# Performance work log

Measured on AMD Instinct MI355X. Metric: run time of the kernel, lower is better.

Reference implementation:

```python
import jax, jax.numpy as jnp
import numpy as np

N = 100000      # nodes
E = 1600000     # edges (before self-loops)
F_IN = 128      # nfeat
H = 64          # nhid
C = 40          # nclass
EPS = 1e-12     # F.normalize eps


def setup_inputs() -> dict:
    key = jax.random.key(0)
    ks = jax.random.split(key, 7)
    x = jax.random.normal(ks[0], (N, F_IN), dtype=jnp.float32)
    edge_index = jax.random.randint(ks[1], (2, E), 0, N, dtype=jnp.int64)
    edge_weight = jax.random.uniform(ks[2], (E,), dtype=jnp.float32)
    # glorot-uniform linear weights (PyG GCNConv default), zero bias
    s1 = float(np.sqrt(6.0 / (F_IN + H)))
    s2 = float(np.sqrt(6.0 / (H + C)))
    W1 = jax.random.uniform(ks[3], (F_IN, H), minval=-s1, maxval=s1, dtype=jnp.float32)
    b1 = jnp.zeros((H,), jnp.float32)
    W2 = jax.random.uniform(ks[4], (H, C), minval=-s2, maxval=s2, dtype=jnp.float32)
    b2 = jnp.zeros((C,), jnp.float32)
    return {"x": x, "edge_index": edge_index, "edge_weight": edge_weight,
            "W1": W1, "b1": b1, "W2": W2, "b2": b2}


def reference(x, edge_index, edge_weight, W1, b1, W2, b2):
    # add self-loops with weight 1 (add_self_loops=True)
    loop = jnp.arange(N, dtype=edge_index.dtype)
    src = jnp.concatenate([edge_index[0], loop])
    dst = jnp.concatenate([edge_index[1], loop])
    ew = jnp.concatenate([edge_weight, jnp.ones((N,), edge_weight.dtype)])
    # symmetric gcn normalization: deg over targets, norm = d^-1/2[src]*w*d^-1/2[dst]
    deg = jax.ops.segment_sum(ew, dst, num_segments=N)
    dinv = jnp.where(deg > 0, jax.lax.rsqrt(jnp.maximum(deg, 1e-30)), 0.0)
    norm = dinv[src] * ew * dinv[dst]

    def conv(h, W, b):
        h = h @ W                                   # [N, out]
        msg = norm[:, None] * h[src]                # gather + scale  [E', out]
        return jax.ops.segment_sum(msg, dst, num_segments=N) + b

    h = jax.nn.relu(conv(x, W1, b1))
    # dropout is identity in eval mode
    h = conv(h, W2, b2)
    # F.normalize(p=2, dim=-1)
    nrm = jnp.linalg.norm(h, axis=-1, keepdims=True)
    return h / jnp.maximum(nrm, EPS)
```

## Files before the change

### kernel.cpp

```cpp
#include <hip/hip_runtime.h>

constexpr int N_ = 100000;
constexpr int E_ = 1600000;
constexpr int FIN = 128;
constexpr int FH  = 64;
constexpr int FC  = 40;
constexpr int KMAX = 64;
constexpr int G1_ROWS = 32;
constexpr float FIXS  = 8388608.0f;
constexpr float FIXSI = 1.0f / 8388608.0f;
constexpr float Q15I  = 1.0f / 32767.0f;

__device__ __forceinline__ float bf2f(unsigned short u) {
  return __uint_as_float((unsigned)u << 16);
}
__device__ __forceinline__ unsigned short f2bf(float f) {
  unsigned b = __float_as_uint(f);
  return (unsigned short)((b + 0x7fffu + ((b >> 16) & 1u)) >> 16);
}


__global__ __launch_bounds__(256) void k_deg_gemm(const int* __restrict__ ei,
                                                  const float* __restrict__ ew,
                                                  unsigned long long* __restrict__ packed,
                                                  unsigned int* __restrict__ csr_pad,
                                                  const float* __restrict__ x,
                                                  const float* __restrict__ W1,
                                                  float* __restrict__ h1) {
  __shared__ ushort4 Wsb[FIN * 16];
  __shared__ float4  xs4[G1_ROWS * 32];
  int bid = blockIdx.x, t = threadIdx.x;
  int r2 = bid & 1, q2 = bid >> 1;
  if (r2 == 0) {
    int e0 = q2 * 512 + t, e1 = e0 + 256;
    int s0 = ei[e0], d0 = ei[E_ + e0];
    int s1 = ei[e1], d1 = ei[E_ + e1];
    float w0 = ew[e0], w1 = ew[e1];
    unsigned int fx0 = (unsigned int)(w0 * FIXS + 0.5f);
    unsigned int fx1 = (unsigned int)(w1 * FIXS + 0.5f);
    unsigned long long old0 =
        atomicAdd(&packed[d0], (1ULL << 32) | (unsigned long long)fx0);
    unsigned long long old1 =
        atomicAdd(&packed[d1], (1ULL << 32) | (unsigned long long)fx1);
    int rank0 = (int)(old0 >> 32), rank1 = (int)(old1 >> 32);
    unsigned int q15a = (unsigned int)(w0 * 32767.0f + 0.5f);
    unsigned int q15b = (unsigned int)(w1 * 32767.0f + 0.5f);
    if (rank0 < KMAX)
      csr_pad[(size_t)d0 * KMAX + rank0] = ((unsigned int)s0 << 15) | q15a;
    if (rank1 < KMAX)
      csr_pad[(size_t)d1 * KMAX + rank1] = ((unsigned int)s1 << 15) | q15b;
    return;
  }
  const float4* W14 = (const float4*)W1;
  const float4* x4  = (const float4*)x;
  int base = q2 * G1_ROWS;
  #pragma unroll
  for (int i = 0; i < 8; ++i) {
    int idx = t + 256 * i;
    float4 w = W14[idx];
    Wsb[idx] = make_ushort4(f2bf(w.x), f2bf(w.y), f2bf(w.z), f2bf(w.w));
  }
  #pragma unroll
  for (int i = 0; i < 4; ++i) xs4[t + 256 * i] = x4[(size_t)base * 32 + t + 256 * i];
  __syncthreads();
  int cg = t & 15, rg = t >> 4;
  int r0 = rg * 2, r1 = r0 + 1;
  float4 a0{0, 0, 0, 0}, a1{0, 0, 0, 0};
  #pragma unroll 2
  for (int k4 = 0; k4 < 32; ++k4) {
    float4 xa = xs4[r0 * 32 + k4];
    float4 xb = xs4[r1 * 32 + k4];
    ushort4 u0 = Wsb[(k4 * 4 + 0) * 16 + cg];
    ushort4 u1 = Wsb[(k4 * 4 + 1) * 16 + cg];
    ushort4 u2 = Wsb[(k4 * 4 + 2) * 16 + cg];
    ushort4 u3 = Wsb[(k4 * 4 + 3) * 16 + cg];
    float4 w0 = make_float4(bf2f(u0.x), bf2f(u0.y), bf2f(u0.z), bf2f(u0.w));
    float4 w1 = make_float4(bf2f(u1.x), bf2f(u1.y), bf2f(u1.z), bf2f(u1.w));
    float4 w2 = make_float4(bf2f(u2.x), bf2f(u2.y), bf2f(u2.z), bf2f(u2.w));
    float4 w3 = make_float4(bf2f(u3.x), bf2f(u3.y), bf2f(u3.z), bf2f(u3.w));
    a0.x += xa.x * w0.x + xa.y * w1.x + xa.z * w2.x + xa.w * w3.x;
    a0.y += xa.x * w0.y + xa.y * w1.y + xa.z * w2.y + xa.w * w3.y;
    a0.z += xa.x * w0.z + xa.y * w1.z + xa.z * w2.z + xa.w * w3.z;
    a0.w += xa.x * w0.w + xa.y * w1.w + xa.z * w2.w + xa.w * w3.w;
    a1.x += xb.x * w0.x + xb.y * w1.x + xb.z * w2.x + xb.w * w3.x;
    a1.y += xb.x * w0.y + xb.y * w1.y + xb.z * w2.y + xb.w * w3.y;
    a1.z += xb.x * w0.z + xb.y * w1.z + xb.z * w2.z + xb.w * w3.z;
    a1.w += xb.x * w0.w + xb.y * w1.w + xb.z * w2.w + xb.w * w3.w;
  }
  ((float4*)h1)[(size_t)(base + r0) * 16 + cg] = a0;
  ((float4*)h1)[(size_t)(base + r1) * 16 + cg] = a1;
}


__global__ __launch_bounds__(256) void k_prep(const unsigned long long* __restrict__ packed,
                                              const float4* __restrict__ h1,
                                              ushort4* __restrict__ h1s,
                                              float* __restrict__ dinv,
                                              int* __restrict__ cnt) {
  int gid = blockIdx.x * 256 + threadIdx.x;
  int i = gid >> 4;
  unsigned long long p = packed[i];
  float dg = 1.0f + (float)(unsigned int)(p & 0xffffffffu) * FIXSI;
  float di = rsqrtf(dg);
  if ((gid & 15) == 0) {
    dinv[i] = di;
    int c = (int)(p >> 32);
    cnt[i] = c < KMAX ? c : KMAX;
  }
  float4 v = h1[gid];
  h1s[gid] = make_ushort4(f2bf(di * v.x), f2bf(di * v.y),
                          f2bf(di * v.z), f2bf(di * v.w));
}


template <int MODE>
__global__ __launch_bounds__(256) void k_agg(const unsigned short* __restrict__ h,
                                             const float* __restrict__ dinv,
                                             const int* __restrict__ cnt,
                                             const unsigned int* __restrict__ csr,
                                             const float* __restrict__ b1,
                                             unsigned short* __restrict__ outp) {
  int wave = threadIdx.x >> 6, lane = threadIdx.x & 63;
  int i = blockIdx.x * 4 + wave;
  int g = lane >> 4, l = lane & 15;
  int n = cnt[i];
  const unsigned int* row = csr + (size_t)i * KMAX;
  const ushort4* h4 = (const ushort4*)h;
  float4 acc{0, 0, 0, 0};
  int jA = g, jB = g + 4;
  unsigned int mA = (jA < n) ? row[jA] : 0;
  unsigned int mB = (jB < n) ? row[jB] : 0;
  while (jA < n) {
    int jA2 = jA + 8, jB2 = jB + 8;
    unsigned int nA = (jA2 < n) ? row[jA2] : 0;
    unsigned int nB = (jB2 < n) ? row[jB2] : 0;
    {
      float w = (float)(mA & 0x7fffu) * Q15I;
      ushort4 v = h4[(size_t)(mA >> 15) * 16 + l];
      acc.x += w * bf2f(v.x); acc.y += w * bf2f(v.y);
      acc.z += w * bf2f(v.z); acc.w += w * bf2f(v.w);
    }
    if (jB < n) {
      float w = (float)(mB & 0x7fffu) * Q15I;
      ushort4 v = h4[(size_t)(mB >> 15) * 16 + l];
      acc.x += w * bf2f(v.x); acc.y += w * bf2f(v.y);
      acc.z += w * bf2f(v.z); acc.w += w * bf2f(v.w);
    }
    jA = jA2; jB = jB2; mA = nA; mB = nB;
  }
  #pragma unroll
  for (int off = 16; off < 64; off <<= 1) {
    acc.x += __shfl_xor(acc.x, off, 64);
    acc.y += __shfl_xor(acc.y, off, 64);
    acc.z += __shfl_xor(acc.z, off, 64);
    acc.w += __shfl_xor(acc.w, off, 64);
  }
  if (g == 0) {
    float di = dinv[i];
    ushort4 sv = h4[(size_t)i * 16 + l];
    float c0 = di * (acc.x + bf2f(sv.x));
    float c1 = di * (acc.y + bf2f(sv.y));
    float c2 = di * (acc.z + bf2f(sv.z));
    float c3 = di * (acc.w + bf2f(sv.w));
    if (MODE == 1) {
      float4 b = ((const float4*)b1)[l];
      c0 = di * fmaxf(c0 + b.x, 0.f);
      c1 = di * fmaxf(c1 + b.y, 0.f);
      c2 = di * fmaxf(c2 + b.z, 0.f);
      c3 = di * fmaxf(c3 + b.w, 0.f);
    }
    ((ushort4*)outp)[(size_t)i * 16 + l] =
        make_ushort4(f2bf(c0), f2bf(c1), f2bf(c2), f2bf(c3));
  }
}


__global__ __launch_bounds__(256) void k_out(const unsigned short* __restrict__ hagg,
                                             const float* __restrict__ W2,
                                             const float* __restrict__ b2,
                                             float* __restrict__ out) {
  __shared__ float WsT[FC * 68];
  __shared__ float hs[4][4 * 68];
  int t = threadIdx.x;
  for (int idx = t; idx < FC * FH; idx += 256) {
    int c = idx >> 6, k = idx & 63;
    WsT[c * 68 + k] = W2[k * FC + c];
  }
  __syncthreads();
  int wave = t >> 6, lane = t & 63;
  int r = lane >> 4, cg = lane & 15;
  int row = blockIdx.x * 16 + wave * 4 + r;
  ushort4 u = ((const ushort4*)hagg)[(size_t)row * 16 + cg];
  float4* hs4 = (float4*)&hs[wave][0];
  hs4[r * 17 + cg] = make_float4(bf2f(u.x), bf2f(u.y), bf2f(u.z), bf2f(u.w));
  const float4* W4T = (const float4*)WsT;
  int c0 = cg, c1 = cg + 16, c2 = cg + 32;
  int c2r = (c2 < FC) ? c2 : 0;
  float a0 = b2[c0], a1 = b2[c1], a2 = (c2 < FC) ? b2[c2] : 0.f;
  #pragma unroll
  for (int kl = 0; kl < 16; ++kl) {
    float4 hk = hs4[r * 17 + kl];
    float4 w0 = W4T[c0 * 17 + kl];
    float4 w1 = W4T[c1 * 17 + kl];
    float4 w2 = W4T[c2r * 17 + kl];
    a0 += hk.x * w0.x + hk.y * w0.y + hk.z * w0.z + hk.w * w0.w;
    a1 += hk.x * w1.x + hk.y * w1.y + hk.z * w1.z + hk.w * w1.w;
    a2 += hk.x * w2.x + hk.y * w2.y + hk.z * w2.z + hk.w * w2.w;
  }
  float sq = a0 * a0 + a1 * a1 + ((c2 < FC) ? a2 * a2 : 0.f);
  #pragma unroll
  for (int off = 1; off < 16; off <<= 1) sq += __shfl_xor(sq, off, 64);
  float inv = 1.0f / fmaxf(sqrtf(sq), 1e-12f);
  float* orow = out + (size_t)row * FC;
  orow[c0] = a0 * inv;
  orow[c1] = a1 * inv;
  if (c2 < FC) orow[c2] = a2 * inv;
}


extern "C" void kernel_launch(void* const* d_in, const int* in_sizes, int n_in,
                              void* d_out, int out_size, void* d_ws, size_t ws_size,
                              hipStream_t stream) {
  const float* x  = (const float*)d_in[0];
  const int*   ei = (const int*)d_in[1];
  const float* ew = (const float*)d_in[2];
  const float* W1 = (const float*)d_in[3];
  const float* b1 = (const float*)d_in[4];
  const float* W2 = (const float*)d_in[5];
  const float* b2 = (const float*)d_in[6];
  float* out = (float*)d_out;

  char* ws = (char*)d_ws;
  size_t off = 0;
  auto alloc = [&](size_t bytes) -> char* {
    char* p = ws + off;
    off = (off + bytes + 255) & ~(size_t)255;
    return p;
  };
  unsigned long long* packed = (unsigned long long*)alloc((size_t)N_ * 8);
  float* dinv    = (float*)alloc((size_t)N_ * 4);
  int*   cnt     = (int*)  alloc((size_t)N_ * 4);
  unsigned int* csr_pad = (unsigned int*)alloc((size_t)N_ * KMAX * 4);
  float* h1      = (float*)alloc((size_t)N_ * FH * 4);
  unsigned short* h1s  = (unsigned short*)alloc((size_t)N_ * FH * 2);
  unsigned short* s2   = (unsigned short*)alloc((size_t)N_ * FH * 2);
  unsigned short* hagg = (unsigned short*)alloc((size_t)N_ * FH * 2);
  (void)ws_size; (void)in_sizes; (void)n_in; (void)out_size;

  hipMemsetAsync(packed, 0, (size_t)N_ * 8, stream);
  k_deg_gemm<<<6250, 256, 0, stream>>>(ei, ew, packed, csr_pad, x, W1, h1);
  k_prep    <<<N_ * 16 / 256, 256, 0, stream>>>(packed, (const float4*)h1,
                                                (ushort4*)h1s, dinv, cnt);
  k_agg<1>  <<<N_ / 4, 256, 0, stream>>>(h1s, dinv, cnt, csr_pad, b1, s2);
  k_agg<2>  <<<N_ / 4, 256, 0, stream>>>(s2, dinv, cnt, csr_pad, nullptr, hagg);
  k_out     <<<N_ / 16, 256, 0, stream>>>(hagg, W2, b2, out);
}
```

Baseline: 241.4 us.

## Pack degree atomics into 32 bits, unroll aggregation 4-way, rewrite output GEMM with shuffles

```diff
diff --git a/kernel.cpp b/kernel.cpp
--- a/kernel.cpp
+++ b/kernel.cpp
@@ -7,9 +7,9 @@
 constexpr int FC  = 40;
 constexpr int KMAX = 64;
 constexpr int G1_ROWS = 32;
-constexpr float FIXS  = 8388608.0f;
-constexpr float FIXSI = 1.0f / 8388608.0f;
-constexpr float Q15I  = 1.0f / 32767.0f;
+constexpr float FIX18  = 262144.0f;
+constexpr float FIX18I = 1.0f / 262144.0f;
+constexpr float Q15I   = 1.0f / 32767.0f;
 
 __device__ __forceinline__ float bf2f(unsigned short u) {
   return __uint_as_float((unsigned)u << 16);
@@ -22,7 +22,7 @@
 
 __global__ __launch_bounds__(256) void k_deg_gemm(const int* __restrict__ ei,
                                                   const float* __restrict__ ew,
-                                                  unsigned long long* __restrict__ packed,
+                                                  unsigned int* __restrict__ packed32,
                                                   unsigned int* __restrict__ csr_pad,
                                                   const float* __restrict__ x,
                                                   const float* __restrict__ W1,
@@ -36,13 +36,11 @@
     int s0 = ei[e0], d0 = ei[E_ + e0];
     int s1 = ei[e1], d1 = ei[E_ + e1];
     float w0 = ew[e0], w1 = ew[e1];
-    unsigned int fx0 = (unsigned int)(w0 * FIXS + 0.5f);
-    unsigned int fx1 = (unsigned int)(w1 * FIXS + 0.5f);
-    unsigned long long old0 =
-        atomicAdd(&packed[d0], (1ULL << 32) | (unsigned long long)fx0);
-    unsigned long long old1 =
-        atomicAdd(&packed[d1], (1ULL << 32) | (unsigned long long)fx1);
-    int rank0 = (int)(old0 >> 32), rank1 = (int)(old1 >> 32);
+    unsigned int fx0 = (unsigned int)(w0 * FIX18 + 0.5f);
+    unsigned int fx1 = (unsigned int)(w1 * FIX18 + 0.5f);
+    unsigned int old0 = atomicAdd(&packed32[d0], (1u << 25) | fx0);
+    unsigned int old1 = atomicAdd(&packed32[d1], (1u << 25) | fx1);
+    int rank0 = (int)(old0 >> 25), rank1 = (int)(old1 >> 25);
     unsigned int q15a = (unsigned int)(w0 * 32767.0f + 0.5f);
     unsigned int q15b = (unsigned int)(w1 * 32767.0f + 0.5f);
     if (rank0 < KMAX)
@@ -92,19 +90,19 @@
 }
 
 
-__global__ __launch_bounds__(256) void k_prep(const unsigned long long* __restrict__ packed,
+__global__ __launch_bounds__(256) void k_prep(const unsigned int* __restrict__ packed32,
                                               const float4* __restrict__ h1,
                                               ushort4* __restrict__ h1s,
                                               float* __restrict__ dinv,
                                               int* __restrict__ cnt) {
   int gid = blockIdx.x * 256 + threadIdx.x;
   int i = gid >> 4;
-  unsigned long long p = packed[i];
-  float dg = 1.0f + (float)(unsigned int)(p & 0xffffffffu) * FIXSI;
+  unsigned int p = packed32[i];
+  float dg = 1.0f + (float)(p & 0x1FFFFFFu) * FIX18I;
   float di = rsqrtf(dg);
   if ((gid & 15) == 0) {
     dinv[i] = di;
-    int c = (int)(p >> 32);
+    int c = (int)(p >> 25);
     cnt[i] = c < KMAX ? c : KMAX;
   }
   float4 v = h1[gid];
@@ -127,13 +125,17 @@
   const unsigned int* row = csr + (size_t)i * KMAX;
   const ushort4* h4 = (const ushort4*)h;
   float4 acc{0, 0, 0, 0};
-  int jA = g, jB = g + 4;
+  int jA = g, jB = g + 4, jC = g + 8, jD = g + 12;
   unsigned int mA = (jA < n) ? row[jA] : 0;
   unsigned int mB = (jB < n) ? row[jB] : 0;
+  unsigned int mC = (jC < n) ? row[jC] : 0;
+  unsigned int mD = (jD < n) ? row[jD] : 0;
   while (jA < n) {
-    int jA2 = jA + 8, jB2 = jB + 8;
+    int jA2 = jA + 16, jB2 = jB + 16, jC2 = jC + 16, jD2 = jD + 16;
     unsigned int nA = (jA2 < n) ? row[jA2] : 0;
     unsigned int nB = (jB2 < n) ? row[jB2] : 0;
+    unsigned int nC = (jC2 < n) ? row[jC2] : 0;
+    unsigned int nD = (jD2 < n) ? row[jD2] : 0;
     {
       float w = (float)(mA & 0x7fffu) * Q15I;
       ushort4 v = h4[(size_t)(mA >> 15) * 16 + l];
@@ -146,7 +148,20 @@
       acc.x += w * bf2f(v.x); acc.y += w * bf2f(v.y);
       acc.z += w * bf2f(v.z); acc.w += w * bf2f(v.w);
     }
-    jA = jA2; jB = jB2; mA = nA; mB = nB;
+    if (jC < n) {
+      float w = (float)(mC & 0x7fffu) * Q15I;
+      ushort4 v = h4[(size_t)(mC >> 15) * 16 + l];
+      acc.x += w * bf2f(v.x); acc.y += w * bf2f(v.y);
+      acc.z += w * bf2f(v.z); acc.w += w * bf2f(v.w);
+    }
+    if (jD < n) {
+      float w = (float)(mD & 0x7fffu) * Q15I;
+      ushort4 v = h4[(size_t)(mD >> 15) * 16 + l];
+      acc.x += w * bf2f(v.x); acc.y += w * bf2f(v.y);
+      acc.z += w * bf2f(v.z); acc.w += w * bf2f(v.w);
+    }
+    jA = jA2; jB = jB2; jC = jC2; jD = jD2;
+    mA = nA; mB = nB; mC = nC; mD = nD;
   }
   #pragma unroll
   for (int off = 16; off < 64; off <<= 1) {
@@ -179,42 +194,40 @@
                                              const float* __restrict__ W2,
                                              const float* __restrict__ b2,
                                              float* __restrict__ out) {
-  __shared__ float WsT[FC * 68];
-  __shared__ float hs[4][4 * 68];
-  int t = threadIdx.x;
-  for (int idx = t; idx < FC * FH; idx += 256) {
-    int c = idx >> 6, k = idx & 63;
-    WsT[c * 68 + k] = W2[k * FC + c];
-  }
-  __syncthreads();
-  int wave = t >> 6, lane = t & 63;
-  int r = lane >> 4, cg = lane & 15;
-  int row = blockIdx.x * 16 + wave * 4 + r;
-  ushort4 u = ((const ushort4*)hagg)[(size_t)row * 16 + cg];
-  float4* hs4 = (float4*)&hs[wave][0];
-  hs4[r * 17 + cg] = make_float4(bf2f(u.x), bf2f(u.y), bf2f(u.z), bf2f(u.w));
-  const float4* W4T = (const float4*)WsT;
-  int c0 = cg, c1 = cg + 16, c2 = cg + 32;
-  int c2r = (c2 < FC) ? c2 : 0;
-  float a0 = b2[c0], a1 = b2[c1], a2 = (c2 < FC) ? b2[c2] : 0.f;
-  #pragma unroll
-  for (int kl = 0; kl < 16; ++kl) {
-    float4 hk = hs4[r * 17 + kl];
-    float4 w0 = W4T[c0 * 17 + kl];
-    float4 w1 = W4T[c1 * 17 + kl];
-    float4 w2 = W4T[c2r * 17 + kl];
-    a0 += hk.x * w0.x + hk.y * w0.y + hk.z * w0.z + hk.w * w0.w;
-    a1 += hk.x * w1.x + hk.y * w1.y + hk.z * w1.z + hk.w * w1.w;
-    a2 += hk.x * w2.x + hk.y * w2.y + hk.z * w2.z + hk.w * w2.w;
-  }
-  float sq = a0 * a0 + a1 * a1 + ((c2 < FC) ? a2 * a2 : 0.f);
-  #pragma unroll
-  for (int off = 1; off < 16; off <<= 1) sq += __shfl_xor(sq, off, 64);
-  float inv = 1.0f / fmaxf(sqrtf(sq), 1e-12f);
-  float* orow = out + (size_t)row * FC;
-  orow[c0] = a0 * inv;
-  orow[c1] = a1 * inv;
-  if (c2 < FC) orow[c2] = a2 * inv;
+  int wave = threadIdx.x >> 6, lane = threadIdx.x & 63;
+  int c = lane;
+  bool live = c < FC;
+  float wcol[64];
+  #pragma unroll
+  for (int k = 0; k < 64; ++k)
+    wcol[k] = live ? W2[k * FC + c] : 0.f;
+  float myb = live ? b2[c] : 0.f;
+  const ushort4* h4 = (const ushort4*)hagg;
+  int base = blockIdx.x * 32 + wave * 8;
+  for (int m = 0; m < 8; ++m) {
+    int i = base + m;
+    ushort4 hv = (lane < 16) ? h4[(size_t)i * 16 + lane]
+                             : make_ushort4(0, 0, 0, 0);
+    unsigned p0 = ((unsigned)hv.y << 16) | hv.x;
+    unsigned p1 = ((unsigned)hv.w << 16) | hv.z;
+    float a = myb;
+    #pragma unroll
+    for (int kk = 0; kk < 16; ++kk) {
+      unsigned q0 = (unsigned)__shfl((int)p0, kk, 64);
+      unsigned q1 = (unsigned)__shfl((int)p1, kk, 64);
+      float h0 = __uint_as_float(q0 << 16);
+      float h1 = __uint_as_float(q0 & 0xffff0000u);
+      float h2 = __uint_as_float(q1 << 16);
+      float h3 = __uint_as_float(q1 & 0xffff0000u);
+      a += h0 * wcol[4 * kk]     + h1 * wcol[4 * kk + 1]
+         + h2 * wcol[4 * kk + 2] + h3 * wcol[4 * kk + 3];
+    }
+    float sq = live ? a * a : 0.f;
+    #pragma unroll
+    for (int off = 1; off < 64; off <<= 1) sq += __shfl_xor(sq, off, 64);
+    float inv = 1.0f / fmaxf(sqrtf(sq), 1e-12f);
+    if (live) out[(size_t)i * FC + c] = a * inv;
+  }
 }
 
 
@@ -237,7 +250,7 @@
     off = (off + bytes + 255) & ~(size_t)255;
     return p;
   };
-  unsigned long long* packed = (unsigned long long*)alloc((size_t)N_ * 8);
+  unsigned int* packed32 = (unsigned int*)alloc((size_t)N_ * 4);
   float* dinv    = (float*)alloc((size_t)N_ * 4);
   int*   cnt     = (int*)  alloc((size_t)N_ * 4);
   unsigned int* csr_pad = (unsigned int*)alloc((size_t)N_ * KMAX * 4);
@@ -247,11 +260,11 @@
   unsigned short* hagg = (unsigned short*)alloc((size_t)N_ * FH * 2);
   (void)ws_size; (void)in_sizes; (void)n_in; (void)out_size;
 
-  hipMemsetAsync(packed, 0, (size_t)N_ * 8, stream);
-  k_deg_gemm<<<6250, 256, 0, stream>>>(ei, ew, packed, csr_pad, x, W1, h1);
-  k_prep    <<<N_ * 16 / 256, 256, 0, stream>>>(packed, (const float4*)h1,
+  hipMemsetAsync(packed32, 0, (size_t)N_ * 4, stream);
+  k_deg_gemm<<<6250, 256, 0, stream>>>(ei, ew, packed32, csr_pad, x, W1, h1);
+  k_prep    <<<N_ * 16 / 256, 256, 0, stream>>>(packed32, (const float4*)h1,
                                                 (ushort4*)h1s, dinv, cnt);
   k_agg<1>  <<<N_ / 4, 256, 0, stream>>>(h1s, dinv, cnt, csr_pad, b1, s2);
   k_agg<2>  <<<N_ / 4, 256, 0, stream>>>(s2, dinv, cnt, csr_pad, nullptr, hagg);
-  k_out     <<<N_ / 16, 256, 0, stream>>>(hagg, W2, b2, out);
-}
+  k_out     <<<N_ / 32, 256, 0, stream>>>(hagg, W2, b2, out);
+}
```

Result: no change. 243.6 us (+0.9%).
